# Optimization experiments

Measured on AMD Instinct MI355X. Metric: run time of the kernel, lower is better.

## Reference

```python
import jax, jax.numpy as jnp
import numpy as np

NUM_HEADS = 16
D_MODEL = 1024
MASK_VALUE = -1000000.0


def setup_inputs() -> dict:
    key = jax.random.key(0)
    ks = jax.random.split(key, 8)
    B, S, D = 2, 2048, D_MODEL
    scale = 1.0 / np.sqrt(D)
    return {
        "queries": jax.random.normal(ks[0], (B, S, D), dtype=jnp.float32),
        "keys": jax.random.normal(ks[1], (B, S, D), dtype=jnp.float32),
        "values": jax.random.normal(ks[2], (B, S, D), dtype=jnp.float32),
        "valid_lens": jax.random.randint(ks[3], (B,), 1, S + 1),
        # Linear weights stored as (in, out); no bias (bias=False)
        "Wq": jax.random.normal(ks[4], (D, D), dtype=jnp.float32) * scale,
        "Wk": jax.random.normal(ks[5], (D, D), dtype=jnp.float32) * scale,
        "Wv": jax.random.normal(ks[6], (D, D), dtype=jnp.float32) * scale,
        "Wo": jax.random.normal(ks[7], (D, D), dtype=jnp.float32) * scale,
    }


def reference(queries, keys, values, valid_lens, Wq, Wk, Wv, Wo):
    B, Sq, D = queries.shape
    Sk = keys.shape[1]
    H = NUM_HEADS
    hd = D // H

    def split_heads(x, S):
        # (B, S, D) -> (B, H, S, hd)
        return x.reshape(B, S, H, hd).transpose(0, 2, 1, 3)

    q = split_heads(queries @ Wq, Sq)
    k = split_heads(keys @ Wk, Sk)
    v = split_heads(values @ Wv, Sk)

    # Faithful to original bug: d_k = queries.size(0) after head-flattening = B*H
    scale = 1.0 / jnp.sqrt(jnp.float32(B * H))
    scores = jnp.einsum("bhqd,bhkd->bhqk", q, k) * scale  # (B,H,Sq,Sk)

    # sequence_mask over last dim, per batch row (valid_lens repeated per head)
    mask = jnp.arange(Sk)[None, None, None, :] < valid_lens[:, None, None, None]
    scores = jnp.where(mask, scores, MASK_VALUE)
    attn = jax.nn.softmax(scores, axis=-1)

    out = jnp.einsum("bhqk,bhkd->bhqd", attn, v)  # (B,H,Sq,hd)
    out = out.transpose(0, 2, 1, 3).reshape(B, Sq, D)
    return out @ Wo
```

## Files before the change

### kernel.cpp

```cpp
#include <hip/hip_runtime.h>
#include <stdint.h>

#define NH 16
#define SEQ 2048
#define DMODEL 1024
#define HD 64
#define NBATCH 2
#define MTOT (NBATCH * SEQ)
#define QSCALE 0.17677669529663687f
#define LOG2E 1.4426950408889634f

typedef __bf16 bf16x8 __attribute__((ext_vector_type(8)));
typedef float f32x4 __attribute__((ext_vector_type(4)));
typedef float f32x16 __attribute__((ext_vector_type(16)));
typedef unsigned uint4v __attribute__((ext_vector_type(4)));

__device__ __forceinline__ unsigned short bf16u(float x) {
  unsigned u = __builtin_bit_cast(unsigned, x);
  u += 0x7fffu + ((u >> 16) & 1u);
  return (unsigned short)(u >> 16);
}

__device__ __forceinline__ float exp2_fast(float x) {
  float r;
  asm("v_exp_f32 %0, %1" : "=v"(r) : "v"(x));
  return r;
}

__device__ __forceinline__ f32x4 mfma16(bf16x8 a, bf16x8 b, f32x4 c) {
  return __builtin_amdgcn_mfma_f32_16x16x32_bf16(a, b, c, 0, 0, 0);
}
__device__ __forceinline__ f32x16 mfma32(bf16x8 a, bf16x8 b, f32x16 c) {
  return __builtin_amdgcn_mfma_f32_32x32x16_bf16(a, b, c, 0, 0, 0);
}

__device__ __forceinline__ void gl16(const void* g, void* l) {
  __builtin_amdgcn_global_load_lds(
      (const __attribute__((address_space(1))) void*)g,
      (__attribute__((address_space(3))) void*)l, 16, 0, 0);
}

__device__ __forceinline__ unsigned cvtpk(float a, float b) {
  unsigned r;
  asm("v_cvt_pk_bf16_f32 %0, %1, %2" : "=v"(r) : "v"(a), "v"(b));
  return r;
}

__global__ __launch_bounds__(256) void cast_x_kernel(
    const float* __restrict__ x0, const float* __restrict__ x1,
    const float* __restrict__ x2, unsigned short* __restrict__ o0,
    unsigned short* __restrict__ o1, unsigned short* __restrict__ o2) {
  const float* src = (blockIdx.y == 0) ? x0 : (blockIdx.y == 1) ? x1 : x2;
  unsigned short* dst = (blockIdx.y == 0) ? o0 : (blockIdx.y == 1) ? o1 : o2;
  const int n4 = MTOT * DMODEL / 4;
  for (int i = blockIdx.x * blockDim.x + threadIdx.x; i < n4;
       i += gridDim.x * blockDim.x) {
    float4 f = reinterpret_cast<const float4*>(src)[i];
    ushort4 u;
    u.x = bf16u(f.x); u.y = bf16u(f.y); u.z = bf16u(f.z); u.w = bf16u(f.w);
    reinterpret_cast<ushort4*>(dst)[i] = u;
  }
}

__global__ __launch_bounds__(256) void transpose_w_kernel(
    const float* __restrict__ w0, const float* __restrict__ w1,
    const float* __restrict__ w2, const float* __restrict__ w3,
    unsigned short* __restrict__ t0, unsigned short* __restrict__ t1,
    unsigned short* __restrict__ t2, unsigned short* __restrict__ t3) {
  __shared__ float tile[64][65];
  const float* w = (blockIdx.z == 0) ? w0 : (blockIdx.z == 1) ? w1
                   : (blockIdx.z == 2) ? w2 : w3;
  unsigned short* t = (blockIdx.z == 0) ? t0 : (blockIdx.z == 1) ? t1
                      : (blockIdx.z == 2) ? t2 : t3;
  const float scl = (blockIdx.z == 0) ? QSCALE * LOG2E : 1.0f;
  int k0 = blockIdx.y * 64, n0 = blockIdx.x * 64;
  int tx = threadIdx.x & 63, ty = threadIdx.x >> 6;
#pragma unroll
  for (int i = 0; i < 16; ++i) {
    int kk = ty * 16 + i;
    tile[kk][tx] = w[(k0 + kk) * DMODEL + n0 + tx];
  }
  __syncthreads();
#pragma unroll
  for (int i = 0; i < 16; ++i) {
    int nn = ty * 16 + i;
    t[(n0 + nn) * DMODEL + k0 + tx] = bf16u(tile[tx][nn] * scl);
  }
}

__global__ __launch_bounds__(256) void gemm_qkv_kernel(
    const unsigned short* __restrict__ xq, const unsigned short* __restrict__ xk,
    const unsigned short* __restrict__ xv,
    const unsigned short* __restrict__ wq, const unsigned short* __restrict__ wk,
    const unsigned short* __restrict__ wv,
    unsigned short* __restrict__ qb, unsigned short* __restrict__ kb,
    unsigned short* __restrict__ vb) {
  __shared__ unsigned short lA[2][128 * 32];
  __shared__ unsigned short lB[2][128 * 32];
  const int z = blockIdx.z;
  const unsigned short* A = (z == 0) ? xq : (z == 1) ? xk : xv;
  const unsigned short* Wt = (z == 0) ? wq : (z == 1) ? wk : wv;
  unsigned short* outb = (z == 0) ? qb : (z == 1) ? kb : vb;

  const int tid = threadIdx.x;
  const int lane = tid & 63, wid = tid >> 6;
  const int wr = wid >> 1, wc = wid & 1;
  const int m0 = blockIdx.x * 128, n0 = blockIdx.y * 128;
  const int lm = lane & 15, lg = lane >> 4;
  const int lk = lg * 8;

  auto stage = [&](int buf, int kt) {
#pragma unroll
    for (int i = 0; i < 2; ++i) {
      int c = tid + i * 256;
      int row = c >> 2, cb = c & 3;
      gl16(A + (m0 + row) * DMODEL + kt * 32 + cb * 8, (char*)lA[buf] + c * 16);
      gl16(Wt + (n0 + row) * DMODEL + kt * 32 + cb * 8, (char*)lB[buf] + c * 16);
    }
  };

  f32x4 acc[4][4] = {};
  stage(0, 0);
  __syncthreads();
  int cur = 0;

  for (int kt = 0; kt < DMODEL / 32; ++kt) {
    if (kt + 1 < DMODEL / 32) stage(cur ^ 1, kt + 1);

    bf16x8 af[4], bfr[4];
#pragma unroll
    for (int x = 0; x < 4; ++x) {
      af[x] = *reinterpret_cast<const bf16x8*>(&lA[cur][(wr * 64 + x * 16 + lm) * 32 + lk]);
      bfr[x] = *reinterpret_cast<const bf16x8*>(&lB[cur][(wc * 64 + x * 16 + lm) * 32 + lk]);
    }
#pragma unroll
    for (int mi = 0; mi < 4; ++mi)
#pragma unroll
      for (int ni = 0; ni < 4; ++ni)
        acc[mi][ni] = mfma16(af[mi], bfr[ni], acc[mi][ni]);

    if (kt + 1 < DMODEL / 32) { __syncthreads(); cur ^= 1; }
  }

#pragma unroll
  for (int mi = 0; mi < 4; ++mi)
#pragma unroll
    for (int ni = 0; ni < 4; ++ni) {
      int col = n0 + wc * 64 + ni * 16 + lm;
#pragma unroll
      for (int r = 0; r < 4; ++r) {
        int row = m0 + wr * 64 + mi * 16 + lg * 4 + r;
        int b = row >> 11, s = row & (SEQ - 1);
        int h = col >> 6, d = col & (HD - 1);
        outb[(((b * NH + h) * SEQ + s) * HD + d)] = bf16u(acc[mi][ni][r]);
      }
    }
}

__global__ __launch_bounds__(256) void gemm_out_kernel(
    const unsigned short* __restrict__ A, const unsigned short* __restrict__ Wt,
    float* __restrict__ outf) {
  __shared__ unsigned short lA[2][128 * 32];
  __shared__ unsigned short lB[2][64 * 32];
  const int tid = threadIdx.x;
  const int lane = tid & 63, wr = tid >> 6;
  const int m0 = blockIdx.x * 128, n0 = blockIdx.y * 64;
  const int lm = lane & 15, lg = lane >> 4;
  const int lk = lg * 8;

  auto stage = [&](int buf, int kt) {
#pragma unroll
    for (int i = 0; i < 2; ++i) {
      int c = tid + i * 256;
      int row = c >> 2, cb = c & 3;
      gl16(A + (m0 + row) * DMODEL + kt * 32 + cb * 8, (char*)lA[buf] + c * 16);
    }
    int c = tid;
    int row = c >> 2, cb = c & 3;
    gl16(Wt + (n0 + row) * DMODEL + kt * 32 + cb * 8, (char*)lB[buf] + c * 16);
  };

  f32x4 acc[2][4] = {};
  stage(0, 0);
  __syncthreads();
  int cur = 0;

  for (int kt = 0; kt < DMODEL / 32; ++kt) {
    if (kt + 1 < DMODEL / 32) stage(cur ^ 1, kt + 1);

    bf16x8 af[2], bfr[4];
#pragma unroll
    for (int x = 0; x < 2; ++x)
      af[x] = *reinterpret_cast<const bf16x8*>(&lA[cur][(wr * 32 + x * 16 + lm) * 32 + lk]);
#pragma unroll
    for (int x = 0; x < 4; ++x)
      bfr[x] = *reinterpret_cast<const bf16x8*>(&lB[cur][(x * 16 + lm) * 32 + lk]);
#pragma unroll
    for (int mi = 0; mi < 2; ++mi)
#pragma unroll
      for (int ni = 0; ni < 4; ++ni)
        acc[mi][ni] = mfma16(af[mi], bfr[ni], acc[mi][ni]);

    if (kt + 1 < DMODEL / 32) { __syncthreads(); cur ^= 1; }
  }

#pragma unroll
  for (int mi = 0; mi < 2; ++mi)
#pragma unroll
    for (int ni = 0; ni < 4; ++ni) {
      int col = n0 + ni * 16 + lm;
#pragma unroll
      for (int r = 0; r < 4; ++r) {
        int row = m0 + wr * 32 + mi * 16 + lg * 4 + r;
        outf[row * DMODEL + col] = acc[mi][ni][r];
      }
    }
}

__global__ __launch_bounds__(256, 2) void attn9_kernel(
    const unsigned short* __restrict__ qb, const unsigned short* __restrict__ kb,
    const unsigned short* __restrict__ vb, const int* __restrict__ vlens,
    unsigned short* __restrict__ ao) {
  __shared__ char klds[4][2][8192];
  const int lane = threadIdx.x & 63;
  const int w = threadIdx.x >> 6;
  const int qi = lane & 31, hi = lane >> 5;
  const int wid = blockIdx.x * 4 + w;
  const int bhi = wid & 31;
  const int chunk = wid >> 5;
  const int b = bhi & 1, h = bhi >> 1;
  const int bh = b * NH + h;
  const int s0w = chunk * 32;
  const int vlen = vlens[b];
  const int nkt = (vlen + 63) >> 6;

  const unsigned short* kbase = kb + bh * SEQ * HD;
  const unsigned short* vbase = vb + (size_t)bh * SEQ * HD;

  const unsigned short* qrow = qb + (bh * SEQ + s0w + qi) * HD;
  bf16x8 qf[4];
#pragma unroll
  for (int ks = 0; ks < 4; ++ks)
    qf[ks] = *reinterpret_cast<const bf16x8*>(qrow + ks * 16 + hi * 8);

  f32x16 oacc[2] = {};
  float m = -3e38f, l = 0.f;

  const int srow = lane >> 3;
  const int scol8 = (lane & 7) ^ (srow & 7);
  auto stageK = [&](int buf, int kt) {
    int k0 = kt * 64;
    char* dst = &klds[w][buf][0];
#pragma unroll
    for (int i = 0; i < 8; ++i)
      gl16(kbase + (size_t)(k0 + i * 8 + srow) * HD + scol8 * 8,
           dst + i * 1024);
  };

  auto readK = [&](bf16x8* kr, int buf) {
    const char* base = &klds[w][buf][0];
#pragma unroll
    for (int kb2 = 0; kb2 < 2; ++kb2)
#pragma unroll
      for (int ks = 0; ks < 4; ++ks) {
        int row = kb2 * 32 + qi;
        int off = row * 128 + ((ks * 32 + hi * 16) ^ ((qi & 7) << 4));
        kr[kb2 * 4 + ks] = *reinterpret_cast<const bf16x8*>(base + off);
      }
  };

  auto body = [&](int t, int buf) {
    const int k0 = t * 64;
    const bool lastt = (t == nkt - 1);

    asm volatile("s_waitcnt vmcnt(0)" ::: "memory");
    __builtin_amdgcn_sched_barrier(0);

    bf16x8 kr[8];
    readK(kr, buf);

    f32x16 s0 = {}, s1 = {};
    __builtin_amdgcn_s_setprio(1);
#pragma unroll
    for (int ks = 0; ks < 4; ++ks) s0 = mfma32(kr[ks], qf[ks], s0);
#pragma unroll
    for (int ks = 0; ks < 4; ++ks) s1 = mfma32(kr[4 + ks], qf[ks], s1);
    __builtin_amdgcn_s_setprio(0);

    if (!lastt) stageK(buf ^ 1, t + 1);

    bf16x8 vr[8];
#pragma unroll
    for (int db = 0; db < 2; ++db)
#pragma unroll
      for (int f = 0; f < 4; ++f) {
        const unsigned short* vp =
            vbase + (size_t)(k0 + f * 16 + 4 * hi) * HD + db * 32 + qi;
        bf16x8 tv;
#pragma unroll
        for (int j = 0; j < 8; ++j) {
          int koff = ((j & 3) + 8 * (j >> 2)) * HD;
          tv[j] = *reinterpret_cast<const __bf16*>(vp + koff);
        }
        vr[db * 4 + f] = tv;
      }

    if (lastt) {
#pragma unroll
      for (int r = 0; r < 16; ++r) {
        int key = k0 + (r & 3) + 8 * (r >> 2) + 4 * hi;
        if (key >= vlen) s0[r] = -1.4426950e6f;
        if (key + 32 >= vlen) s1[r] = -1.4426950e6f;
      }
    }

    float mx8[8];
#pragma unroll
    for (int i = 0; i < 8; ++i)
      mx8[i] = fmaxf(fmaxf(s0[i], s0[i + 8]), fmaxf(s1[i], s1[i + 8]));
#pragma unroll
    for (int st = 4; st; st >>= 1)
#pragma unroll
      for (int i = 0; i < st; ++i) mx8[i] = fmaxf(mx8[i], mx8[i + st]);
    float mx = fmaxf(mx8[0], __shfl_xor(mx8[0], 32, 64));
    float mn = fmaxf(m, mx);
    float sf = exp2_fast(m - mn);
    m = mn;

#pragma unroll
    for (int r = 0; r < 16; ++r) s0[r] = exp2_fast(s0[r] - mn);
#pragma unroll
    for (int r = 0; r < 16; ++r) s1[r] = exp2_fast(s1[r] - mn);
    float sm8[8];
#pragma unroll
    for (int i = 0; i < 8; ++i)
      sm8[i] = (s0[i] + s0[i + 8]) + (s1[i] + s1[i + 8]);
#pragma unroll
    for (int st = 4; st; st >>= 1)
#pragma unroll
      for (int i = 0; i < st; ++i) sm8[i] += sm8[i + st];
    float ps = sm8[0] + __shfl_xor(sm8[0], 32, 64);
    l = l * sf + ps;
#pragma unroll
    for (int db = 0; db < 2; ++db) oacc[db] *= sf;

    bf16x8 pf[4];
    auto packP = [&](const f32x16& s, bf16x8* out) {
#pragma unroll
      for (int f = 0; f < 2; ++f) {
        uint4v wv;
#pragma unroll
        for (int k2 = 0; k2 < 4; ++k2)
          wv[k2] = cvtpk(s[f * 8 + k2 * 2], s[f * 8 + k2 * 2 + 1]);
        out[f] = __builtin_bit_cast(bf16x8, wv);
      }
    };
    packP(s0, pf);
    packP(s1, pf + 2);

    __builtin_amdgcn_s_setprio(1);
#pragma unroll
    for (int db = 0; db < 2; ++db)
#pragma unroll
      for (int f = 0; f < 4; ++f)
        oacc[db] = mfma32(vr[db * 4 + f], pf[f], oacc[db]);
    __builtin_amdgcn_s_setprio(0);
  };

  stageK(0, 0);
  for (int t = 0; t < nkt; ++t) body(t, t & 1);

  const float linv = 1.0f / l;
#pragma unroll
  for (int db = 0; db < 2; ++db)
#pragma unroll
    for (int rq = 0; rq < 4; ++rq) {
      ushort4 o;
      o.x = bf16u(oacc[db][rq * 4 + 0] * linv);
      o.y = bf16u(oacc[db][rq * 4 + 1] * linv);
      o.z = bf16u(oacc[db][rq * 4 + 2] * linv);
      o.w = bf16u(oacc[db][rq * 4 + 3] * linv);
      int d = db * 32 + 8 * rq + 4 * hi;
      *reinterpret_cast<ushort4*>(
          ao + (b * SEQ + s0w + qi) * DMODEL + h * HD + d) = o;
    }
}

extern "C" void kernel_launch(void* const* d_in, const int* in_sizes, int n_in,
                              void* d_out, int out_size, void* d_ws, size_t ws_size,
                              hipStream_t stream) {
  (void)in_sizes; (void)n_in; (void)out_size; (void)ws_size;
  const float* q = (const float*)d_in[0];
  const float* k = (const float*)d_in[1];
  const float* v = (const float*)d_in[2];
  const int* vlens = (const int*)d_in[3];
  const float* Wq = (const float*)d_in[4];
  const float* Wk = (const float*)d_in[5];
  const float* Wv = (const float*)d_in[6];
  const float* Wo = (const float*)d_in[7];
  float* out = (float*)d_out;

  char* ws = (char*)d_ws;
  const size_t MB = 1u << 20;
  unsigned short* xq = (unsigned short*)(ws + 0 * MB);
  unsigned short* xk = (unsigned short*)(ws + 8 * MB);
  unsigned short* xv = (unsigned short*)(ws + 16 * MB);
  unsigned short* wqt = (unsigned short*)(ws + 24 * MB);
  unsigned short* wkt = (unsigned short*)(ws + 26 * MB);
  unsigned short* wvt = (unsigned short*)(ws + 28 * MB);
  unsigned short* wot = (unsigned short*)(ws + 30 * MB);
  unsigned short* qb = (unsigned short*)(ws + 32 * MB);
  unsigned short* kb = (unsigned short*)(ws + 40 * MB);
  unsigned short* vb = (unsigned short*)(ws + 48 * MB);
  unsigned short* ao = (unsigned short*)(ws + 56 * MB);

  cast_x_kernel<<<dim3(512, 3), 256, 0, stream>>>(q, k, v, xq, xk, xv);
  transpose_w_kernel<<<dim3(16, 16, 4), 256, 0, stream>>>(Wq, Wk, Wv, Wo,
                                                          wqt, wkt, wvt, wot);
  gemm_qkv_kernel<<<dim3(32, 8, 3), 256, 0, stream>>>(xq, xk, xv, wqt, wkt, wvt,
                                                      qb, kb, vb);
  attn9_kernel<<<dim3(512), 256, 0, stream>>>(qb, kb, vb, vlens, ao);
  gemm_out_kernel<<<dim3(32, 16), 256, 0, stream>>>(ao, wot, out);
}
```

Before: 120.5 us.

## Share K/V tiles across block waves and store V transposed for LDS reads

```diff
diff --git a/kernel.cpp b/kernel.cpp
--- a/kernel.cpp
+++ b/kernel.cpp
@@ -14,6 +14,8 @@
 typedef float f32x4 __attribute__((ext_vector_type(4)));
 typedef float f32x16 __attribute__((ext_vector_type(16)));
 typedef unsigned uint4v __attribute__((ext_vector_type(4)));
+typedef unsigned long long u64;
+struct u64x2 { u64 lo, hi; };
 
 __device__ __forceinline__ unsigned short bf16u(float x) {
   unsigned u = __builtin_bit_cast(unsigned, x);
@@ -45,6 +47,7 @@
   asm("v_cvt_pk_bf16_f32 %0, %1, %2" : "=v"(r) : "v"(a), "v"(b));
   return r;
 }
+
 
 __global__ __launch_bounds__(256) void cast_x_kernel(
     const float* __restrict__ x0, const float* __restrict__ x1,
@@ -94,13 +97,14 @@
     const unsigned short* __restrict__ wq, const unsigned short* __restrict__ wk,
     const unsigned short* __restrict__ wv,
     unsigned short* __restrict__ qb, unsigned short* __restrict__ kb,
-    unsigned short* __restrict__ vb) {
+    unsigned short* __restrict__ vt) {
   __shared__ unsigned short lA[2][128 * 32];
   __shared__ unsigned short lB[2][128 * 32];
   const int z = blockIdx.z;
   const unsigned short* A = (z == 0) ? xq : (z == 1) ? xk : xv;
   const unsigned short* Wt = (z == 0) ? wq : (z == 1) ? wk : wv;
-  unsigned short* outb = (z == 0) ? qb : (z == 1) ? kb : vb;
+  unsigned short* outb = (z == 0) ? qb : (z == 1) ? kb : vt;
+  const int mode = (z == 2) ? 1 : 0;
 
   const int tid = threadIdx.x;
   const int lane = tid & 63, wid = tid >> 6;
@@ -152,7 +156,9 @@
         int row = m0 + wr * 64 + mi * 16 + lg * 4 + r;
         int b = row >> 11, s = row & (SEQ - 1);
         int h = col >> 6, d = col & (HD - 1);
-        outb[(((b * NH + h) * SEQ + s) * HD + d)] = bf16u(acc[mi][ni][r]);
+        int idx = (mode == 0) ? (((b * NH + h) * SEQ + s) * HD + d)
+                              : (((b * NH + h) * HD + d) * SEQ + s);
+        outb[idx] = bf16u(acc[mi][ni][r]);
       }
     }
 }
@@ -217,27 +223,28 @@
     }
 }
 
-__global__ __launch_bounds__(256, 2) void attn9_kernel(
+__global__ __launch_bounds__(256) void attn13_kernel(
     const unsigned short* __restrict__ qb, const unsigned short* __restrict__ kb,
-    const unsigned short* __restrict__ vb, const int* __restrict__ vlens,
+    const unsigned short* __restrict__ vt, const int* __restrict__ vlens,
     unsigned short* __restrict__ ao) {
-  __shared__ char klds[4][2][8192];
+  __shared__ char klds[2][8192];
+  __shared__ char vlds[2][8192];
   const int lane = threadIdx.x & 63;
   const int w = threadIdx.x >> 6;
   const int qi = lane & 31, hi = lane >> 5;
-  const int wid = blockIdx.x * 4 + w;
-  const int bhi = wid & 31;
-  const int chunk = wid >> 5;
+  const int bid = blockIdx.x;
+  const int bhi = bid & 31;
+  const int chunk = bid >> 5;
   const int b = bhi & 1, h = bhi >> 1;
   const int bh = b * NH + h;
-  const int s0w = chunk * 32;
+  const int s0b = chunk * 128;
   const int vlen = vlens[b];
   const int nkt = (vlen + 63) >> 6;
 
   const unsigned short* kbase = kb + bh * SEQ * HD;
-  const unsigned short* vbase = vb + (size_t)bh * SEQ * HD;
-
-  const unsigned short* qrow = qb + (bh * SEQ + s0w + qi) * HD;
+  const unsigned short* vtb = vt + (size_t)bh * HD * SEQ;
+
+  const unsigned short* qrow = qb + (bh * SEQ + s0b + w * 32 + qi) * HD;
   bf16x8 qf[4];
 #pragma unroll
   for (int ks = 0; ks < 4; ++ks)
@@ -248,36 +255,36 @@
 
   const int srow = lane >> 3;
   const int scol8 = (lane & 7) ^ (srow & 7);
-  auto stageK = [&](int buf, int kt) {
+  auto stage = [&](int buf, int kt) {
     int k0 = kt * 64;
-    char* dst = &klds[w][buf][0];
-#pragma unroll
-    for (int i = 0; i < 8; ++i)
+#pragma unroll
+    for (int ii = 0; ii < 2; ++ii) {
+      int i = w * 2 + ii;
       gl16(kbase + (size_t)(k0 + i * 8 + srow) * HD + scol8 * 8,
-           dst + i * 1024);
-  };
-
-  auto readK = [&](bf16x8* kr, int buf) {
-    const char* base = &klds[w][buf][0];
-#pragma unroll
-    for (int kb2 = 0; kb2 < 2; ++kb2)
-#pragma unroll
-      for (int ks = 0; ks < 4; ++ks) {
-        int row = kb2 * 32 + qi;
-        int off = row * 128 + ((ks * 32 + hi * 16) ^ ((qi & 7) << 4));
-        kr[kb2 * 4 + ks] = *reinterpret_cast<const bf16x8*>(base + off);
-      }
+           &klds[buf][i * 1024]);
+      gl16(vtb + (size_t)(i * 8 + srow) * SEQ + k0 + scol8 * 8,
+           &vlds[buf][i * 1024]);
+    }
   };
 
   auto body = [&](int t, int buf) {
     const int k0 = t * 64;
     const bool lastt = (t == nkt - 1);
 
-    asm volatile("s_waitcnt vmcnt(0)" ::: "memory");
-    __builtin_amdgcn_sched_barrier(0);
+    if (!lastt) stage(buf ^ 1, t + 1);
 
     bf16x8 kr[8];
-    readK(kr, buf);
+    {
+      const char* base = &klds[buf][0];
+#pragma unroll
+      for (int kb2 = 0; kb2 < 2; ++kb2)
+#pragma unroll
+        for (int ks = 0; ks < 4; ++ks) {
+          int row = kb2 * 32 + qi;
+          int off = row * 128 + ((ks * 32 + hi * 16) ^ ((row & 7) << 4));
+          kr[kb2 * 4 + ks] = *reinterpret_cast<const bf16x8*>(base + off);
+        }
+    }
 
     f32x16 s0 = {}, s1 = {};
     __builtin_amdgcn_s_setprio(1);
@@ -287,23 +294,21 @@
     for (int ks = 0; ks < 4; ++ks) s1 = mfma32(kr[4 + ks], qf[ks], s1);
     __builtin_amdgcn_s_setprio(0);
 
-    if (!lastt) stageK(buf ^ 1, t + 1);
-
     bf16x8 vr[8];
-#pragma unroll
-    for (int db = 0; db < 2; ++db)
-#pragma unroll
-      for (int f = 0; f < 4; ++f) {
-        const unsigned short* vp =
-            vbase + (size_t)(k0 + f * 16 + 4 * hi) * HD + db * 32 + qi;
-        bf16x8 tv;
-#pragma unroll
-        for (int j = 0; j < 8; ++j) {
-          int koff = ((j & 3) + 8 * (j >> 2)) * HD;
-          tv[j] = *reinterpret_cast<const __bf16*>(vp + koff);
+    {
+      const char* base = &vlds[buf][0];
+#pragma unroll
+      for (int db = 0; db < 2; ++db)
+#pragma unroll
+        for (int f = 0; f < 4; ++f) {
+          int r = db * 32 + qi;
+          int sw = (r & 7) << 4;
+          int c = f * 32 + hi * 8;
+          u64 lo = *reinterpret_cast<const u64*>(base + r * 128 + (c ^ sw));
+          u64 hi8 = *reinterpret_cast<const u64*>(base + r * 128 + ((c + 16) ^ sw));
+          vr[db * 4 + f] = __builtin_bit_cast(bf16x8, u64x2{lo, hi8});
         }
-        vr[db * 4 + f] = tv;
-      }
+    }
 
     if (lastt) {
 #pragma unroll
@@ -365,10 +370,18 @@
       for (int f = 0; f < 4; ++f)
         oacc[db] = mfma32(vr[db * 4 + f], pf[f], oacc[db]);
     __builtin_amdgcn_s_setprio(0);
+
+    if (!lastt) {
+      asm volatile("s_waitcnt vmcnt(0)" ::: "memory");
+      __syncthreads();
+    }
   };
 
-  stageK(0, 0);
-  for (int t = 0; t < nkt; ++t) body(t, t & 1);
+  stage(0, 0);
+  asm volatile("s_waitcnt vmcnt(0)" ::: "memory");
+  __syncthreads();
+  int buf = 0;
+  for (int t = 0; t < nkt; ++t) { body(t, buf); buf ^= 1; }
 
   const float linv = 1.0f / l;
 #pragma unroll
@@ -382,7 +395,7 @@
       o.w = bf16u(oacc[db][rq * 4 + 3] * linv);
       int d = db * 32 + 8 * rq + 4 * hi;
       *reinterpret_cast<ushort4*>(
-          ao + (b * SEQ + s0w + qi) * DMODEL + h * HD + d) = o;
+          ao + (b * SEQ + s0b + w * 32 + qi) * DMODEL + h * HD + d) = o;
     }
 }
 
@@ -411,14 +424,14 @@
   unsigned short* wot = (unsigned short*)(ws + 30 * MB);
   unsigned short* qb = (unsigned short*)(ws + 32 * MB);
   unsigned short* kb = (unsigned short*)(ws + 40 * MB);
-  unsigned short* vb = (unsigned short*)(ws + 48 * MB);
+  unsigned short* vt = (unsigned short*)(ws + 48 * MB);
   unsigned short* ao = (unsigned short*)(ws + 56 * MB);
 
   cast_x_kernel<<<dim3(512, 3), 256, 0, stream>>>(q, k, v, xq, xk, xv);
   transpose_w_kernel<<<dim3(16, 16, 4), 256, 0, stream>>>(Wq, Wk, Wv, Wo,
                                                           wqt, wkt, wvt, wot);
   gemm_qkv_kernel<<<dim3(32, 8, 3), 256, 0, stream>>>(xq, xk, xv, wqt, wkt, wvt,
-                                                      qb, kb, vb);
-  attn9_kernel<<<dim3(512), 256, 0, stream>>>(qb, kb, vb, vlens, ao);
+                                                      qb, kb, vt);
+  attn13_kernel<<<dim3(512), 256, 0, stream>>>(qb, kb, vt, vlens, ao);
   gemm_out_kernel<<<dim3(32, 16), 256, 0, stream>>>(ao, wot, out);
 }
```

Result: slower. 133.8 us (+11.0%).

## Fuse prep kernels and double-buffer V register prefetch in attention

Applied to the files above, without the earlier changes.

```diff
diff --git a/kernel.cpp b/kernel.cpp
--- a/kernel.cpp
+++ b/kernel.cpp
@@ -46,45 +46,49 @@
   return r;
 }
 
-__global__ __launch_bounds__(256) void cast_x_kernel(
+
+__global__ __launch_bounds__(256) void prep_kernel(
     const float* __restrict__ x0, const float* __restrict__ x1,
     const float* __restrict__ x2, unsigned short* __restrict__ o0,
-    unsigned short* __restrict__ o1, unsigned short* __restrict__ o2) {
-  const float* src = (blockIdx.y == 0) ? x0 : (blockIdx.y == 1) ? x1 : x2;
-  unsigned short* dst = (blockIdx.y == 0) ? o0 : (blockIdx.y == 1) ? o1 : o2;
-  const int n4 = MTOT * DMODEL / 4;
-  for (int i = blockIdx.x * blockDim.x + threadIdx.x; i < n4;
-       i += gridDim.x * blockDim.x) {
-    float4 f = reinterpret_cast<const float4*>(src)[i];
-    ushort4 u;
-    u.x = bf16u(f.x); u.y = bf16u(f.y); u.z = bf16u(f.z); u.w = bf16u(f.w);
-    reinterpret_cast<ushort4*>(dst)[i] = u;
-  }
-}
-
-__global__ __launch_bounds__(256) void transpose_w_kernel(
+    unsigned short* __restrict__ o1, unsigned short* __restrict__ o2,
     const float* __restrict__ w0, const float* __restrict__ w1,
     const float* __restrict__ w2, const float* __restrict__ w3,
     unsigned short* __restrict__ t0, unsigned short* __restrict__ t1,
     unsigned short* __restrict__ t2, unsigned short* __restrict__ t3) {
-  __shared__ float tile[64][65];
-  const float* w = (blockIdx.z == 0) ? w0 : (blockIdx.z == 1) ? w1
-                   : (blockIdx.z == 2) ? w2 : w3;
-  unsigned short* t = (blockIdx.z == 0) ? t0 : (blockIdx.z == 1) ? t1
-                      : (blockIdx.z == 2) ? t2 : t3;
-  const float scl = (blockIdx.z == 0) ? QSCALE * LOG2E : 1.0f;
-  int k0 = blockIdx.y * 64, n0 = blockIdx.x * 64;
-  int tx = threadIdx.x & 63, ty = threadIdx.x >> 6;
-#pragma unroll
-  for (int i = 0; i < 16; ++i) {
-    int kk = ty * 16 + i;
-    tile[kk][tx] = w[(k0 + kk) * DMODEL + n0 + tx];
-  }
-  __syncthreads();
-#pragma unroll
-  for (int i = 0; i < 16; ++i) {
-    int nn = ty * 16 + i;
-    t[(n0 + nn) * DMODEL + k0 + tx] = bf16u(tile[tx][nn] * scl);
+  const int id = blockIdx.x;
+  if (id < 1536) {
+    const int src = id >> 9, blk = id & 511;
+    const float* s = (src == 0) ? x0 : (src == 1) ? x1 : x2;
+    unsigned short* d = (src == 0) ? o0 : (src == 1) ? o1 : o2;
+    const int n4 = MTOT * DMODEL / 4;
+    for (int i = blk * 256 + threadIdx.x; i < n4; i += 512 * 256) {
+      float4 f = reinterpret_cast<const float4*>(s)[i];
+      ushort4 u;
+      u.x = bf16u(f.x); u.y = bf16u(f.y); u.z = bf16u(f.z); u.w = bf16u(f.w);
+      reinterpret_cast<ushort4*>(d)[i] = u;
+    }
+  } else {
+    __shared__ float tile[64][65];
+    const int id2 = id - 1536;
+    const int wsel = id2 >> 8, tl = id2 & 255;
+    const float* w = (wsel == 0) ? w0 : (wsel == 1) ? w1
+                     : (wsel == 2) ? w2 : w3;
+    unsigned short* t = (wsel == 0) ? t0 : (wsel == 1) ? t1
+                        : (wsel == 2) ? t2 : t3;
+    const float scl = (wsel == 0) ? QSCALE * LOG2E : 1.0f;
+    int n0 = (tl & 15) * 64, k0 = (tl >> 4) * 64;
+    int tx = threadIdx.x & 63, ty = threadIdx.x >> 6;
+#pragma unroll
+    for (int i = 0; i < 16; ++i) {
+      int kk = ty * 16 + i;
+      tile[kk][tx] = w[(k0 + kk) * DMODEL + n0 + tx];
+    }
+    __syncthreads();
+#pragma unroll
+    for (int i = 0; i < 16; ++i) {
+      int nn = ty * 16 + i;
+      t[(n0 + nn) * DMODEL + k0 + tx] = bf16u(tile[tx][nn] * scl);
+    }
   }
 }
 
@@ -217,7 +221,7 @@
     }
 }
 
-__global__ __launch_bounds__(256, 2) void attn9_kernel(
+__global__ __launch_bounds__(256) void attn14_kernel(
     const unsigned short* __restrict__ qb, const unsigned short* __restrict__ kb,
     const unsigned short* __restrict__ vb, const int* __restrict__ vlens,
     unsigned short* __restrict__ ao) {
@@ -269,27 +273,8 @@
       }
   };
 
-  auto body = [&](int t, int buf) {
-    const int k0 = t * 64;
-    const bool lastt = (t == nkt - 1);
-
-    asm volatile("s_waitcnt vmcnt(0)" ::: "memory");
-    __builtin_amdgcn_sched_barrier(0);
-
-    bf16x8 kr[8];
-    readK(kr, buf);
-
-    f32x16 s0 = {}, s1 = {};
-    __builtin_amdgcn_s_setprio(1);
-#pragma unroll
-    for (int ks = 0; ks < 4; ++ks) s0 = mfma32(kr[ks], qf[ks], s0);
-#pragma unroll
-    for (int ks = 0; ks < 4; ++ks) s1 = mfma32(kr[4 + ks], qf[ks], s1);
-    __builtin_amdgcn_s_setprio(0);
-
-    if (!lastt) stageK(buf ^ 1, t + 1);
-
-    bf16x8 vr[8];
+  auto loadV = [&](bf16x8* vr, int kt) {
+    int k0 = kt * 64;
 #pragma unroll
     for (int db = 0; db < 2; ++db)
 #pragma unroll
@@ -304,6 +289,30 @@
         }
         vr[db * 4 + f] = tv;
       }
+  };
+
+  auto body = [&](int t, int buf, bf16x8* vrCur, bf16x8* vrNext, int tn) {
+    const int k0 = t * 64;
+    const bool lastt = (t == nkt - 1);
+
+    asm volatile("s_waitcnt vmcnt(0)" ::: "memory");
+    __builtin_amdgcn_sched_barrier(0);
+
+    bf16x8 kr[8];
+    readK(kr, buf);
+
+    f32x16 s0 = {}, s1 = {};
+    __builtin_amdgcn_s_setprio(1);
+#pragma unroll
+    for (int ks = 0; ks < 4; ++ks) s0 = mfma32(kr[ks], qf[ks], s0);
+#pragma unroll
+    for (int ks = 0; ks < 4; ++ks) s1 = mfma32(kr[4 + ks], qf[ks], s1);
+    __builtin_amdgcn_s_setprio(0);
+
+    if (!lastt) {
+      stageK(buf ^ 1, tn);
+      loadV(vrNext, tn);
+    }
 
     if (lastt) {
 #pragma unroll
@@ -363,12 +372,18 @@
     for (int db = 0; db < 2; ++db)
 #pragma unroll
       for (int f = 0; f < 4; ++f)
-        oacc[db] = mfma32(vr[db * 4 + f], pf[f], oacc[db]);
+        oacc[db] = mfma32(vrCur[db * 4 + f], pf[f], oacc[db]);
     __builtin_amdgcn_s_setprio(0);
   };
 
+  bf16x8 vrA[8], vrB[8];
   stageK(0, 0);
-  for (int t = 0; t < nkt; ++t) body(t, t & 1);
+  loadV(vrA, 0);
+  for (int t = 0; t < nkt; t += 2) {
+    body(t, 0, vrA, vrB, t + 1);
+    if (t + 1 >= nkt) break;
+    body(t + 1, 1, vrB, vrA, t + 2);
+  }
 
   const float linv = 1.0f / l;
 #pragma unroll
@@ -414,11 +429,11 @@
   unsigned short* vb = (unsigned short*)(ws + 48 * MB);
   unsigned short* ao = (unsigned short*)(ws + 56 * MB);
 
-  cast_x_kernel<<<dim3(512, 3), 256, 0, stream>>>(q, k, v, xq, xk, xv);
-  transpose_w_kernel<<<dim3(16, 16, 4), 256, 0, stream>>>(Wq, Wk, Wv, Wo,
-                                                          wqt, wkt, wvt, wot);
+  prep_kernel<<<dim3(2560), 256, 0, stream>>>(q, k, v, xq, xk, xv,
+                                              Wq, Wk, Wv, Wo,
+                                              wqt, wkt, wvt, wot);
   gemm_qkv_kernel<<<dim3(32, 8, 3), 256, 0, stream>>>(xq, xk, xv, wqt, wkt, wvt,
                                                       qb, kb, vb);
-  attn9_kernel<<<dim3(512), 256, 0, stream>>>(qb, kb, vb, vlens, ao);
+  attn14_kernel<<<dim3(512), 256, 0, stream>>>(qb, kb, vb, vlens, ao);
   gemm_out_kernel<<<dim3(32, 16), 256, 0, stream>>>(ao, wot, out);
 }
```

Measured after the change: 163.1 us. 1.35x slower.
